# Kernel tuning notes

Measured on AMD Instinct MI355X. Metric: run time of the kernel, lower is better.

Reference implementation:

```python
import jax, jax.numpy as jnp
import numpy as np

IM_SIZE = (32, 32)
SCALE = float(IM_SIZE[0] * IM_SIZE[1])  # sqrt((x*y)^2) = x*y


def setup_inputs() -> dict:
    key = jax.random.key(0)
    k1, k2, k3 = jax.random.split(key, 3)
    b, n, p, x, y, d = 8, 8, 64, IM_SIZE[0], IM_SIZE[1], 8
    shape = (b, n, p, x, y, d)
    return {
        "query": jax.random.normal(k1, shape, dtype=jnp.float32),
        "key": jax.random.normal(k2, shape, dtype=jnp.float32),
        "value": jax.random.normal(k3, shape, dtype=jnp.float32),
        "key_padding_mask": jnp.zeros((b, p), dtype=bool),
    }


def reference(query, key, value, key_padding_mask):
    # scores: contract over spatial (x,y) and channel (d) dims -> [b,n,p,q]
    scores = jnp.einsum('bnpxyd,bnqxyd->bnpq', query, key) / SCALE
    if key_padding_mask is not None:
        mask = key_padding_mask[:, None, None, :]  # [b,1,1,q]
        scores = jnp.where(mask, -jnp.inf, scores)
    attn = jax.nn.softmax(scores, axis=-1)  # [b,n,p,q]
    out = jnp.einsum('bnpq,bnqxyd->bnpxyd', attn, value)
    # permute(0,2,3,4,5,1) -> [b,p,x,y,d,n]
    return jnp.transpose(out, (0, 2, 3, 4, 5, 1))
```

## Files before the change

kernel.cpp:

```cpp
#include <hip/hip_runtime.h>
#include <hip/hip_bf16.h>
#include <cstdint>
#include <cstddef>


typedef __attribute__((ext_vector_type(4))) float f32x4;
typedef __attribute__((ext_vector_type(8))) short bf16x8;
typedef __attribute__((ext_vector_type(4))) short shortx4;

__device__ __forceinline__ unsigned short f2bf(float x) {
    unsigned int u = __builtin_bit_cast(unsigned int, x);
    u += 0x7FFFu + ((u >> 16) & 1u);
    return (unsigned short)(u >> 16);
}

__device__ __forceinline__ bf16x8 pack8(float4 lo, float4 hi) {
    bf16x8 f;
    f[0] = (short)f2bf(lo.x); f[1] = (short)f2bf(lo.y);
    f[2] = (short)f2bf(lo.z); f[3] = (short)f2bf(lo.w);
    f[4] = (short)f2bf(hi.x); f[5] = (short)f2bf(hi.y);
    f[6] = (short)f2bf(hi.z); f[7] = (short)f2bf(hi.w);
    return f;
}

__global__ __launch_bounds__(256, 4) void qk_mfma_kernel(
    const float* __restrict__ Q, const float* __restrict__ K,
    float* __restrict__ partial, int clen)
{
    const int bn   = blockIdx.x;
    const int ch   = blockIdx.y;
    const int tid  = threadIdx.x;
    const int w    = tid >> 6;
    const int lane = tid & 63;
    const int wr   = w >> 1;
    const int wc   = w & 1;
    const int frow = lane & 15;
    const int kg   = lane >> 4;

    const float* Qb = Q + (size_t)bn * 64 * 8192 + (size_t)ch * clen;
    const float* Kb = K + (size_t)bn * 64 * 8192 + (size_t)ch * clen;
    const float* Aq = Qb + (size_t)(wr * 32 + frow) * 8192 + kg * 8;
    const float* Bk = Kb + (size_t)(wc * 32 + frow) * 8192 + kg * 8;

    const int nsteps = clen >> 5;

    f32x4 acc[2][2];
    #pragma unroll
    for (int mt = 0; mt < 2; ++mt)
        #pragma unroll
        for (int nt = 0; nt < 2; ++nt)
            acc[mt][nt] = (f32x4)(0.f);

#define LOADSTEP(buf, stp) do {                                              \
        const int _s  = (stp);                                               \
        const int _ks = (_s < nsteps ? _s : nsteps - 1) * 32;                \
        buf[0] = *(const float4*)(Aq + _ks);                                 \
        buf[1] = *(const float4*)(Aq + _ks + 4);                             \
        buf[2] = *(const float4*)(Aq + 16 * 8192 + _ks);                     \
        buf[3] = *(const float4*)(Aq + 16 * 8192 + _ks + 4);                 \
        buf[4] = *(const float4*)(Bk + _ks);                                 \
        buf[5] = *(const float4*)(Bk + _ks + 4);                             \
        buf[6] = *(const float4*)(Bk + 16 * 8192 + _ks);                     \
        buf[7] = *(const float4*)(Bk + 16 * 8192 + _ks + 4);                 \
    } while (0)

#define COMPUTESTEP(buf) do {                                                \
        const bf16x8 a0 = pack8(buf[0], buf[1]);                             \
        const bf16x8 a1 = pack8(buf[2], buf[3]);                             \
        const bf16x8 b0 = pack8(buf[4], buf[5]);                             \
        const bf16x8 b1 = pack8(buf[6], buf[7]);                             \
        acc[0][0] = __builtin_amdgcn_mfma_f32_16x16x32_bf16(a0, b0, acc[0][0], 0, 0, 0); \
        acc[0][1] = __builtin_amdgcn_mfma_f32_16x16x32_bf16(a0, b1, acc[0][1], 0, 0, 0); \
        acc[1][0] = __builtin_amdgcn_mfma_f32_16x16x32_bf16(a1, b0, acc[1][0], 0, 0, 0); \
        acc[1][1] = __builtin_amdgcn_mfma_f32_16x16x32_bf16(a1, b1, acc[1][1], 0, 0, 0); \
    } while (0)

    float4 bufA[8], bufB[8];
    LOADSTEP(bufA, 0);
    LOADSTEP(bufB, 1);
    #pragma unroll 1
    for (int s = 0; s < nsteps; s += 2) {
        COMPUTESTEP(bufA);
        LOADSTEP(bufA, s + 2);
        COMPUTESTEP(bufB);
        LOADSTEP(bufB, s + 3);
    }
#undef LOADSTEP
#undef COMPUTESTEP

    float* pb = partial + ((size_t)ch * 64 + bn) * 4096;
    #pragma unroll
    for (int mt = 0; mt < 2; ++mt)
        #pragma unroll
        for (int nt = 0; nt < 2; ++nt) {
            const int p0 = wr * 32 + mt * 16 + kg * 4;
            const int q0 = wc * 32 + nt * 16 + frow;
            #pragma unroll
            for (int r = 0; r < 4; ++r)
                pb[(size_t)(p0 + r) * 64 + q0] = acc[mt][nt][r];
        }
}

__global__ __launch_bounds__(256) void softmax_kernel(
    float* __restrict__ ws, const unsigned char* __restrict__ mask, int kchunks)
{
    const int row  = blockIdx.x * 4 + (threadIdx.x >> 6);
    const int q    = threadIdx.x & 63;
    float s = 0.f;
    for (int c = 0; c < kchunks; ++c)
        s += ws[((size_t)c * 4096 + row) * 64 + q];
    s *= (1.0f / 1024.0f);
    const int b = row >> 9;
    if (mask[b * 64 + q]) s = -__builtin_inff();
    float m = s;
    #pragma unroll
    for (int off = 32; off; off >>= 1) m = fmaxf(m, __shfl_xor(m, off));
    const float e = __expf(s - m);
    float sum = e;
    #pragma unroll
    for (int off = 32; off; off >>= 1) sum += __shfl_xor(sum, off);
    ws[(size_t)row * 64 + q] = e / sum;
}

__global__ __launch_bounds__(512, 2) void pv_mfma_kernel(
    const float* __restrict__ V, const float* __restrict__ attn,
    float* __restrict__ out)
{
    __shared__ unsigned char smem[65536];

    const int b     = blockIdx.y;
    const int chunk = blockIdx.x;
    const int tid   = threadIdx.x;
    const int w     = tid >> 6;
    const int lane  = tid & 63;

    const float* Vb = V    + (size_t)(b * 8 + w) * 64 * 8192 + (size_t)chunk * 64;
    const float* Ab = attn + (size_t)(b * 8 + w) * 4096;

    unsigned short* vtn = (unsigned short*)smem + w * 4096;

    const int c  = lane >> 2;
    const int qg = lane & 3;
    #pragma unroll
    for (int s = 0; s < 4; ++s) {
        const int q0 = s * 16 + qg * 4;
        const float4 r0 = *(const float4*)&Vb[(size_t)(q0 + 0) * 8192 + c * 4];
        const float4 r1 = *(const float4*)&Vb[(size_t)(q0 + 1) * 8192 + c * 4];
        const float4 r2 = *(const float4*)&Vb[(size_t)(q0 + 2) * 8192 + c * 4];
        const float4 r3 = *(const float4*)&Vb[(size_t)(q0 + 3) * 8192 + c * 4];
        const float v0[4] = {r0.x, r0.y, r0.z, r0.w};
        const float v1[4] = {r1.x, r1.y, r1.z, r1.w};
        const float v2[4] = {r2.x, r2.y, r2.z, r2.w};
        const float v3[4] = {r3.x, r3.y, r3.z, r3.w};
        #pragma unroll
        for (int cc = 0; cc < 4; ++cc) {
            const int row = c * 4 + cc;
            shortx4 pk;
            pk.x = (short)f2bf(v0[cc]);
            pk.y = (short)f2bf(v1[cc]);
            pk.z = (short)f2bf(v2[cc]);
            pk.w = (short)f2bf(v3[cc]);
            const int soff = row * 64 + (q0 ^ ((row & 7) << 3) ^ (((row >> 3) & 3) << 4));
            *(shortx4*)(vtn + soff) = pk;
        }
    }

    const int arow = lane & 15;
    const int q0a  = (lane >> 4) * 8;
    bf16x8 afrag[4][2];
    #pragma unroll
    for (int mt = 0; mt < 4; ++mt) {
        #pragma unroll
        for (int ks = 0; ks < 2; ++ks) {
            const float* ap = Ab + (mt * 16 + arow) * 64 + ks * 32 + q0a;
            const float4 lo = *(const float4*)ap;
            const float4 hi = *(const float4*)(ap + 4);
            afrag[mt][ks] = pack8(lo, hi);
        }
    }

    f32x4 acc[4][4];
    #pragma unroll
    for (int mt = 0; mt < 4; ++mt)
        #pragma unroll
        for (int nt = 0; nt < 4; ++nt)
            acc[mt][nt] = (f32x4)(0.f);

    const int bcol = lane & 15;
    const int q0b  = (lane >> 4) * 8;
    #pragma unroll
    for (int nt = 0; nt < 4; ++nt) {
        bf16x8 bfr[2];
        #pragma unroll
        for (int ks = 0; ks < 2; ++ks) {
            const int row  = nt * 16 + bcol;
            const int q0   = ks * 32 + q0b;
            const int soff = row * 64 + (q0 ^ ((row & 7) << 3) ^ (((row >> 3) & 3) << 4));
            bfr[ks] = *(const bf16x8*)(vtn + soff);
        }
        #pragma unroll
        for (int ks = 0; ks < 2; ++ks)
            #pragma unroll
            for (int mt = 0; mt < 4; ++mt)
                acc[mt][nt] = __builtin_amdgcn_mfma_f32_16x16x32_bf16(
                    afrag[mt][ks], bfr[ks], acc[mt][nt], 0, 0, 0);
    }

    float* ob = (float*)smem;
    const int pq = lane >> 4;
    const int pl = tid >> 5;
    const int g  = tid & 31;
    #pragma unroll
    for (int mt = 0; mt < 4; ++mt) {
        __syncthreads();
        #pragma unroll
        for (int nt = 0; nt < 4; ++nt)
            #pragma unroll
            for (int r = 0; r < 4; ++r) {
                const int prow = pq * 4 + r;
                const int xc   = nt * 16 + (lane & 15);
                ob[prow * 576 + xc * 9 + w] = acc[mt][nt][r];
            }
        __syncthreads();
        float* orow = out + (size_t)b * 4194304 + (size_t)(mt * 16 + pl) * 65536
                          + (size_t)chunk * 512;
        #pragma unroll
        for (int u = 0; u < 4; ++u) {
            const int f0 = g * 4 + u * 128;
            float4 vv;
            vv.x = ob[pl * 576 + ((f0 + 0) >> 3) * 9 + ((f0 + 0) & 7)];
            vv.y = ob[pl * 576 + ((f0 + 1) >> 3) * 9 + ((f0 + 1) & 7)];
            vv.z = ob[pl * 576 + ((f0 + 2) >> 3) * 9 + ((f0 + 2) & 7)];
            vv.w = ob[pl * 576 + ((f0 + 3) >> 3) * 9 + ((f0 + 3) & 7)];
            *(float4*)&orow[f0] = vv;
        }
    }
}

extern "C" void kernel_launch(void* const* d_in, const int* in_sizes, int n_in,
                              void* d_out, int out_size, void* d_ws, size_t ws_size,
                              hipStream_t stream)
{
    const float* Q = (const float*)d_in[0];
    const float* K = (const float*)d_in[1];
    const float* V = (const float*)d_in[2];
    const unsigned char* mask = (const unsigned char*)d_in[3];
    float* out = (float*)d_out;
    float* ws  = (float*)d_ws;

    int kchunks = 16;
    while (kchunks > 1 &&
           (size_t)kchunks * 4096 * 64 * sizeof(float) > ws_size)
        kchunks >>= 1;
    const int clen = 8192 / kchunks;

    qk_mfma_kernel<<<dim3(64, kchunks), 256, 0, stream>>>(Q, K, ws, clen);
    softmax_kernel<<<1024, 256, 0, stream>>>(ws, mask, kchunks);
    pv_mfma_kernel<<<dim3(128, 8), 512, 0, stream>>>(V, ws, out);
}
```

Before: 142.3 us.

## Stage QK tiles through swizzled LDS with 1024-thread blocks

The QK score kernel now loads each Q and K row once per block, converts it to bf16, and stores it into shared memory with an XOR swizzle. Sixteen waves then read their MFMA fragments from LDS. Before, each row fragment was loaded redundantly from global memory by the two waves that needed it. The split-K chunk count doubles to 32 to keep enough blocks in flight. In exchange, each phase adds two block-wide barriers, register prefetch across phases is lost, and the partial-sum buffer written and read by the softmax kernel doubles in size.

```diff
diff --git a/kernel.cpp b/kernel.cpp
--- a/kernel.cpp
+++ b/kernel.cpp
@@ -23,82 +23,64 @@
     return f;
 }
 
-__global__ __launch_bounds__(256, 4) void qk_mfma_kernel(
+__global__ __launch_bounds__(1024) void qk_mfma_kernel(
     const float* __restrict__ Q, const float* __restrict__ K,
     float* __restrict__ partial, int clen)
 {
+    __shared__ unsigned short Qs[64 * 256];
+    __shared__ unsigned short Ks[64 * 256];
+
     const int bn   = blockIdx.x;
     const int ch   = blockIdx.y;
     const int tid  = threadIdx.x;
     const int w    = tid >> 6;
     const int lane = tid & 63;
-    const int wr   = w >> 1;
-    const int wc   = w & 1;
+    const int wr   = w >> 2;
+    const int wc   = w & 3;
     const int frow = lane & 15;
     const int kg   = lane >> 4;
 
     const float* Qb = Q + (size_t)bn * 64 * 8192 + (size_t)ch * clen;
     const float* Kb = K + (size_t)bn * 64 * 8192 + (size_t)ch * clen;
-    const float* Aq = Qb + (size_t)(wr * 32 + frow) * 8192 + kg * 8;
-    const float* Bk = Kb + (size_t)(wc * 32 + frow) * 8192 + kg * 8;
-
-    const int nsteps = clen >> 5;
-
-    f32x4 acc[2][2];
-    #pragma unroll
-    for (int mt = 0; mt < 2; ++mt)
-        #pragma unroll
-        for (int nt = 0; nt < 2; ++nt)
-            acc[mt][nt] = (f32x4)(0.f);
-
-#define LOADSTEP(buf, stp) do {                                              \
-        const int _s  = (stp);                                               \
-        const int _ks = (_s < nsteps ? _s : nsteps - 1) * 32;                \
-        buf[0] = *(const float4*)(Aq + _ks);                                 \
-        buf[1] = *(const float4*)(Aq + _ks + 4);                             \
-        buf[2] = *(const float4*)(Aq + 16 * 8192 + _ks);                     \
-        buf[3] = *(const float4*)(Aq + 16 * 8192 + _ks + 4);                 \
-        buf[4] = *(const float4*)(Bk + _ks);                                 \
-        buf[5] = *(const float4*)(Bk + _ks + 4);                             \
-        buf[6] = *(const float4*)(Bk + 16 * 8192 + _ks);                     \
-        buf[7] = *(const float4*)(Bk + 16 * 8192 + _ks + 4);                 \
-    } while (0)
-
-#define COMPUTESTEP(buf) do {                                                \
-        const bf16x8 a0 = pack8(buf[0], buf[1]);                             \
-        const bf16x8 a1 = pack8(buf[2], buf[3]);                             \
-        const bf16x8 b0 = pack8(buf[4], buf[5]);                             \
-        const bf16x8 b1 = pack8(buf[6], buf[7]);                             \
-        acc[0][0] = __builtin_amdgcn_mfma_f32_16x16x32_bf16(a0, b0, acc[0][0], 0, 0, 0); \
-        acc[0][1] = __builtin_amdgcn_mfma_f32_16x16x32_bf16(a0, b1, acc[0][1], 0, 0, 0); \
-        acc[1][0] = __builtin_amdgcn_mfma_f32_16x16x32_bf16(a1, b0, acc[1][0], 0, 0, 0); \
-        acc[1][1] = __builtin_amdgcn_mfma_f32_16x16x32_bf16(a1, b1, acc[1][1], 0, 0, 0); \
-    } while (0)
-
-    float4 bufA[8], bufB[8];
-    LOADSTEP(bufA, 0);
-    LOADSTEP(bufB, 1);
+
+    const int srow = tid >> 4;
+    const int sc   = (tid & 15) * 16;
+    const int nph  = clen >> 8;
+
+    f32x4 acc = (f32x4)(0.f);
+    const int arow = wr * 16 + frow;
+    const int brow = wc * 16 + frow;
+
     #pragma unroll 1
-    for (int s = 0; s < nsteps; s += 2) {
-        COMPUTESTEP(bufA);
-        LOADSTEP(bufA, s + 2);
-        COMPUTESTEP(bufB);
-        LOADSTEP(bufB, s + 3);
-    }
-#undef LOADSTEP
-#undef COMPUTESTEP
+    for (int ph = 0; ph < nph; ++ph) {
+        const float4* qp = (const float4*)(Qb + (size_t)srow * 8192 + ph * 256 + sc);
+        const float4* kp = (const float4*)(Kb + (size_t)srow * 8192 + ph * 256 + sc);
+        const float4 q0 = qp[0], q1 = qp[1], q2 = qp[2], q3 = qp[3];
+        const float4 k0 = kp[0], k1 = kp[1], k2 = kp[2], k3 = kp[3];
+        if (ph) __syncthreads();
+        const int sl0 = ((tid & 15) * 2    ) ^ (srow & 7);
+        const int sl1 = ((tid & 15) * 2 + 1) ^ (srow & 7);
+        *(bf16x8*)(Qs + srow * 256 + sl0 * 8) = pack8(q0, q1);
+        *(bf16x8*)(Qs + srow * 256 + sl1 * 8) = pack8(q2, q3);
+        *(bf16x8*)(Ks + srow * 256 + sl0 * 8) = pack8(k0, k1);
+        *(bf16x8*)(Ks + srow * 256 + sl1 * 8) = pack8(k2, k3);
+        __syncthreads();
+        #pragma unroll
+        for (int ks = 0; ks < 8; ++ks) {
+            const bf16x8 a = *(const bf16x8*)(Qs + arow * 256 +
+                                (((ks * 4 + kg) ^ (arow & 7)) * 8));
+            const bf16x8 b = *(const bf16x8*)(Ks + brow * 256 +
+                                (((ks * 4 + kg) ^ (brow & 7)) * 8));
+            acc = __builtin_amdgcn_mfma_f32_16x16x32_bf16(a, b, acc, 0, 0, 0);
+        }
+    }
 
     float* pb = partial + ((size_t)ch * 64 + bn) * 4096;
-    #pragma unroll
-    for (int mt = 0; mt < 2; ++mt)
-        #pragma unroll
-        for (int nt = 0; nt < 2; ++nt) {
-            const int p0 = wr * 32 + mt * 16 + kg * 4;
-            const int q0 = wc * 32 + nt * 16 + frow;
-            #pragma unroll
-            for (int r = 0; r < 4; ++r)
-                pb[(size_t)(p0 + r) * 64 + q0] = acc[mt][nt][r];
-        }
+    const int p0 = wr * 16 + kg * 4;
+    const int q0 = wc * 16 + frow;
+    #pragma unroll
+    for (int r = 0; r < 4; ++r)
+        pb[(size_t)(p0 + r) * 64 + q0] = acc[r];
 }
 
 __global__ __launch_bounds__(256) void softmax_kernel(
@@ -248,13 +230,13 @@
     float* out = (float*)d_out;
     float* ws  = (float*)d_ws;
 
-    int kchunks = 16;
+    int kchunks = 32;
     while (kchunks > 1 &&
            (size_t)kchunks * 4096 * 64 * sizeof(float) > ws_size)
         kchunks >>= 1;
     const int clen = 8192 / kchunks;
 
-    qk_mfma_kernel<<<dim3(64, kchunks), 256, 0, stream>>>(Q, K, ws, clen);
+    qk_mfma_kernel<<<dim3(64, kchunks), 1024, 0, stream>>>(Q, K, ws, clen);
     softmax_kernel<<<1024, 256, 0, stream>>>(ws, mask, kchunks);
     pv_mfma_kernel<<<dim3(128, 8), 512, 0, stream>>>(V, ws, out);
 }
```

New measurement: 141.7 us. No clear change (-0.4%).
